# Kernel optimization log

Hardware: AMD Instinct MI355X
Metric: run time of the kernel (lower is better)

The kernel has to match this reference:

```python
import jax, jax.numpy as jnp
import numpy as np

HEADS = 16
DIM_HEAD = 64


def setup_inputs() -> dict:
    key = jax.random.key(0)
    k1, k2, k3, k4 = jax.random.split(key, 4)
    B, T, D = 4, 1024, 1024
    x = jax.random.normal(k1, (B, T, D), dtype=jnp.float32)
    w_qkv = jax.random.normal(k2, (3 * HEADS * DIM_HEAD, D), dtype=jnp.float32) * (1.0 / np.sqrt(D))
    w_out = jax.random.normal(k3, (D, HEADS * DIM_HEAD), dtype=jnp.float32) * (1.0 / np.sqrt(HEADS * DIM_HEAD))
    rel_bias = jax.random.normal(k4, (2 * 1024 - 1, HEADS), dtype=jnp.float32) * 0.02
    return {"x": x, "w_qkv": w_qkv, "w_out": w_out, "rel_bias": rel_bias}


def reference(x, w_qkv, w_out, rel_bias):
    b, t, _ = x.shape
    h, dh = HEADS, DIM_HEAD
    scale = dh ** (-0.5)
    qkv = x @ w_qkv.T  # [b, t, 3*h*dh]
    # einops 'b t (d k h) -> k b h t d': last axis factors as (dh, 3, h)
    qkv = qkv.reshape(b, t, dh, 3, h).transpose(3, 0, 4, 1, 2)  # [3, b, h, t, dh]
    q, k, v = qkv[0], qkv[1], qkv[2]
    scores = jnp.einsum('bhid,bhjd->bhij', q, k) * scale  # [b, h, t, t]
    # relative position bias: rel[i,j] = j - i + t - 1
    rel = jnp.arange(t)[None, :] - jnp.arange(t)[:, None] + (t - 1)  # [t, t]
    bias = rel_bias[rel]  # [t, t, h]
    scores = scores + bias.transpose(2, 0, 1)[None]  # [b, h, t, t]
    attn = jax.nn.softmax(scores, axis=-1)
    out = jnp.einsum('bhij,bhjd->bhid', attn, v)  # [b, h, t, dh]
    out = out.transpose(0, 2, 1, 3).reshape(b, t, h * dh)  # 'b h t d -> b t (h d)'
    return out @ w_out.T
```

## Files before the change

### kernel.cpp

```cpp
#include <hip/hip_runtime.h>
#include <hip/hip_bf16.h>

typedef short bf16x8 __attribute__((ext_vector_type(8)));
typedef float f32x4  __attribute__((ext_vector_type(4)));

typedef __attribute__((address_space(3))) void lds_t;
typedef __attribute__((address_space(1))) void gbl_t;

#define MFMA16(a,b,c) __builtin_amdgcn_mfma_f32_16x16x32_bf16((a),(b),(c),0,0,0)

__device__ __forceinline__ unsigned short f2bf(float f) {
    __hip_bfloat16 h = __float2bfloat16(f);
    return __builtin_bit_cast(unsigned short, h);
}
__device__ __forceinline__ float bf2f(unsigned short u) {
    __hip_bfloat16 h = __builtin_bit_cast(__hip_bfloat16, u);
    return __bfloat162float(h);
}

__global__ void prep_all(const float* __restrict__ x,
                         const float* __restrict__ w_qkv,
                         const float* __restrict__ w_out,
                         unsigned short* __restrict__ A1h,
                         unsigned short* __restrict__ W1h,
                         unsigned short* __restrict__ W3h) {
    const int NX = 4096 * 256, NW1 = 3072 * 256, NW3 = 1024 * 256;
    for (int idx = blockIdx.x * blockDim.x + threadIdx.x; idx < NX + NW1 + NW3;
         idx += gridDim.x * blockDim.x) {
        if (idx < NX) {
            int base = idx * 4;
            float4 v = *reinterpret_cast<const float4*>(x + base);
            ushort4 hi;
            hi.x = f2bf(v.x); hi.y = f2bf(v.y);
            hi.z = f2bf(v.z); hi.w = f2bf(v.w);
            *reinterpret_cast<ushort4*>(A1h + base) = hi;
        } else if (idx < NX + NW1) {
            int base = (idx - NX) * 4;
            int n = base >> 10, c = base & 1023;
            int d = n & 63, which = n >> 10, h = (n >> 6) & 15;
            int srow = d * 48 + which * 16 + h;
            float4 v =
                *reinterpret_cast<const float4*>(w_qkv + (size_t)srow * 1024 + c);
            ushort4 hi;
            hi.x = f2bf(v.x); hi.y = f2bf(v.y);
            hi.z = f2bf(v.z); hi.w = f2bf(v.w);
            *reinterpret_cast<ushort4*>(W1h + (size_t)n * 1024 + c) = hi;
        } else {
            int base = (idx - NX - NW1) * 4;
            float4 v = *reinterpret_cast<const float4*>(w_out + base);
            ushort4 hi;
            hi.x = f2bf(v.x); hi.y = f2bf(v.y);
            hi.z = f2bf(v.z); hi.w = f2bf(v.w);
            *reinterpret_cast<ushort4*>(W3h + base) = hi;
        }
    }
}

__global__ __launch_bounds__(512, 2) void gemm256_hi(
    const unsigned short* __restrict__ A, const unsigned short* __restrict__ B,
    unsigned short* __restrict__ outQ, unsigned short* __restrict__ outK,
    unsigned short* __restrict__ outV) {
    __shared__ unsigned short lds[65536];
    const int tid = threadIdx.x;
    const int wid = tid >> 6, lane = tid & 63;
    const int lrow = lane & 15, lgrp = lane >> 4;
    const int wr = wid >> 2, wc = wid & 3;
    const int mtile = blockIdx.y * 256, ntile = blockIdx.x * 256;

    const int csw = lgrp ^ ((lrow >> 1) & 3);
    const int aoff = (wr * 128 + lrow) * 32 + csw * 8;
    const int boff = 32768 + (wc * 64 + lrow) * 32 + csw * 8;

    const int sreg = wid * 2;
    const int srow0 = sreg * 16 + (lane >> 2);
    const int srow1 = (sreg + 1) * 16 + (lane >> 2);
    const int schunk = (lane & 3) ^ ((lane >> 3) & 3);
    const int sdst0 = sreg * 512;

    f32x4 acc[8][4];
#pragma unroll
    for (int i = 0; i < 8; ++i)
#pragma unroll
        for (int j = 0; j < 4; ++j) {
            f32x4 z = {0.f, 0.f, 0.f, 0.f};
            acc[i][j] = z;
        }

#pragma unroll
    for (int s0 = 0; s0 < 2; ++s0) {
        const int kb = s0 * 32;
        __builtin_amdgcn_global_load_lds(
            (const gbl_t*)(A + (size_t)(mtile + srow0) * 1024 + kb + schunk * 8),
            (lds_t*)(lds + s0 * 8192 + sdst0), 16, 0, 0);
        __builtin_amdgcn_global_load_lds(
            (const gbl_t*)(A + (size_t)(mtile + srow1) * 1024 + kb + schunk * 8),
            (lds_t*)(lds + s0 * 8192 + sdst0 + 512), 16, 0, 0);
        __builtin_amdgcn_global_load_lds(
            (const gbl_t*)(B + (size_t)(ntile + srow0) * 1024 + kb + schunk * 8),
            (lds_t*)(lds + 32768 + s0 * 8192 + sdst0), 16, 0, 0);
        __builtin_amdgcn_global_load_lds(
            (const gbl_t*)(B + (size_t)(ntile + srow1) * 1024 + kb + schunk * 8),
            (lds_t*)(lds + 32768 + s0 * 8192 + sdst0 + 512), 16, 0, 0);
    }
    asm volatile("s_waitcnt vmcnt(4)" ::: "memory");
    __syncthreads();

    for (int s = 0; s < 32; ++s) {
        const int sa = s & 3;
        const unsigned short* sbase = lds + sa * 8192;

        bf16x8 af[8];
#pragma unroll
        for (int i = 0; i < 8; ++i)
            af[i] = *reinterpret_cast<const bf16x8*>(sbase + aoff + i * 512);
        bf16x8 b0 = *reinterpret_cast<const bf16x8*>(sbase + boff);
        bf16x8 b1 = *reinterpret_cast<const bf16x8*>(sbase + boff + 512);

        if (s <= 29) {
            const int kb2 = (s + 2) * 32;
            const int s2 = (s + 2) & 3;
            __builtin_amdgcn_global_load_lds(
                (const gbl_t*)(A + (size_t)(mtile + srow0) * 1024 + kb2 + schunk * 8),
                (lds_t*)(lds + s2 * 8192 + sdst0), 16, 0, 0);
            __builtin_amdgcn_global_load_lds(
                (const gbl_t*)(A + (size_t)(mtile + srow1) * 1024 + kb2 + schunk * 8),
                (lds_t*)(lds + s2 * 8192 + sdst0 + 512), 16, 0, 0);
        }
        __builtin_amdgcn_s_setprio(1);
#pragma unroll
        for (int i = 0; i < 8; ++i) {
            acc[i][0] = MFMA16(af[i], b0, acc[i][0]);
            acc[i][1] = MFMA16(af[i], b1, acc[i][1]);
        }
        __builtin_amdgcn_s_setprio(0);

        bf16x8 b2 = *reinterpret_cast<const bf16x8*>(sbase + boff + 1024);
        bf16x8 b3 = *reinterpret_cast<const bf16x8*>(sbase + boff + 1536);
        if (s <= 29) {
            const int kb2 = (s + 2) * 32;
            const int s2 = (s + 2) & 3;
            __builtin_amdgcn_global_load_lds(
                (const gbl_t*)(B + (size_t)(ntile + srow0) * 1024 + kb2 + schunk * 8),
                (lds_t*)(lds + 32768 + s2 * 8192 + sdst0), 16, 0, 0);
            __builtin_amdgcn_global_load_lds(
                (const gbl_t*)(B + (size_t)(ntile + srow1) * 1024 + kb2 + schunk * 8),
                (lds_t*)(lds + 32768 + s2 * 8192 + sdst0 + 512), 16, 0, 0);
        }
        __builtin_amdgcn_s_setprio(1);
#pragma unroll
        for (int i = 0; i < 8; ++i) {
            acc[i][2] = MFMA16(af[i], b2, acc[i][2]);
            acc[i][3] = MFMA16(af[i], b3, acc[i][3]);
        }
        __builtin_amdgcn_s_setprio(0);

        if (s < 31) {
            if (s <= 29)
                asm volatile("s_waitcnt vmcnt(4)" ::: "memory");
            else
                asm volatile("s_waitcnt vmcnt(0)" ::: "memory");
            __syncthreads();
        }
    }

#pragma unroll
    for (int i = 0; i < 8; ++i) {
#pragma unroll
        for (int j = 0; j < 4; ++j) {
#pragma unroll
            for (int r = 0; r < 4; ++r) {
                float v = acc[i][j][r];
                int m = mtile + wr * 128 + i * 16 + lgrp * 4 + r;
                int n = ntile + wc * 64 + j * 16 + lrow;
                int which = n >> 10;
                int hh = (n >> 6) & 15;
                int d = n & 63;
                int b = m >> 10, t = m & 1023;
                unsigned short* dstp =
                    (which == 0) ? outQ : ((which == 1) ? outK : outV);
                dstp[((size_t)((b << 4) + hh) * 1024 + t) * 64 + d] = f2bf(v);
            }
        }
    }
}

__global__ __launch_bounds__(256, 3) void gemm_out_v5(
    const unsigned short* __restrict__ A, const unsigned short* __restrict__ B,
    float* __restrict__ outF) {
    __shared__ unsigned short As[2][64 * 64];
    __shared__ unsigned short Bs[2][128 * 64];
    const int tid = threadIdx.x;
    const int wid = tid >> 6, lane = tid & 63;
    const int lrow = lane & 15, lgrp = lane >> 4;
    const int wr = wid >> 1, wc = wid & 1;
    const int h = blockIdx.x;
    const int xcd = h & 7, within = h >> 3;
    const int mtile = (xcd * 8 + (within & 7)) * 64;
    const int ntile = (within >> 3) * 128;

    const int srow = tid >> 3;
    const int schunk = (tid & 7) ^ (srow & 7);
    const unsigned short* Abase = A + (size_t)(mtile + srow) * 1024 + schunk * 8;
    const unsigned short* Bbase = B + (size_t)(ntile + srow) * 1024 + schunk * 8;

    const int csw0 = (lgrp ^ (lrow & 7)) * 8;
    const int csw1 = ((4 | lgrp) ^ (lrow & 7)) * 8;
    const int arow = wr * 32 + lrow;
    const int brow = wc * 64 + lrow;

    f32x4 acc[2][4];
#pragma unroll
    for (int i = 0; i < 2; ++i)
#pragma unroll
        for (int j = 0; j < 4; ++j) {
            f32x4 z = {0.f, 0.f, 0.f, 0.f};
            acc[i][j] = z;
        }

#pragma unroll
    for (int e = 0; e < 2; ++e)
        __builtin_amdgcn_global_load_lds(
            (const gbl_t*)(Abase + (size_t)e * 32 * 1024),
            (lds_t*)(&As[0][0] + e * 2048 + tid * 8), 16, 0, 0);
#pragma unroll
    for (int e = 0; e < 4; ++e)
        __builtin_amdgcn_global_load_lds(
            (const gbl_t*)(Bbase + (size_t)e * 32 * 1024),
            (lds_t*)(&Bs[0][0] + e * 2048 + tid * 8), 16, 0, 0);
    asm volatile("s_waitcnt vmcnt(0)" ::: "memory");
    __syncthreads();

    for (int s = 0; s < 16; ++s) {
        const int cur = s & 1;
        if (s < 15) {
            const int kb = (s + 1) * 64;
            const int nx = cur ^ 1;
#pragma unroll
            for (int e = 0; e < 2; ++e)
                __builtin_amdgcn_global_load_lds(
                    (const gbl_t*)(Abase + (size_t)e * 32 * 1024 + kb),
                    (lds_t*)(&As[nx][0] + e * 2048 + tid * 8), 16, 0, 0);
#pragma unroll
            for (int e = 0; e < 4; ++e)
                __builtin_amdgcn_global_load_lds(
                    (const gbl_t*)(Bbase + (size_t)e * 32 * 1024 + kb),
                    (lds_t*)(&Bs[nx][0] + e * 2048 + tid * 8), 16, 0, 0);
        }
        bf16x8 a0[2], a1[2], b0[4], b1[4];
#pragma unroll
        for (int i = 0; i < 2; ++i) {
            a0[i] = *reinterpret_cast<const bf16x8*>(&As[cur][0] +
                                                     (arow + i * 16) * 64 + csw0);
            a1[i] = *reinterpret_cast<const bf16x8*>(&As[cur][0] +
                                                     (arow + i * 16) * 64 + csw1);
        }
#pragma unroll
        for (int j = 0; j < 4; ++j) {
            b0[j] = *reinterpret_cast<const bf16x8*>(&Bs[cur][0] +
                                                     (brow + j * 16) * 64 + csw0);
            b1[j] = *reinterpret_cast<const bf16x8*>(&Bs[cur][0] +
                                                     (brow + j * 16) * 64 + csw1);
        }
        __builtin_amdgcn_s_setprio(1);
#pragma unroll
        for (int i = 0; i < 2; ++i)
#pragma unroll
            for (int j = 0; j < 4; ++j) {
                acc[i][j] = MFMA16(a0[i], b0[j], acc[i][j]);
                acc[i][j] = MFMA16(a1[i], b1[j], acc[i][j]);
            }
        __builtin_amdgcn_s_setprio(0);
        if (s < 15) {
            asm volatile("s_waitcnt vmcnt(0)" ::: "memory");
            __syncthreads();
        }
    }

#pragma unroll
    for (int i = 0; i < 2; ++i)
#pragma unroll
        for (int j = 0; j < 4; ++j)
#pragma unroll
            for (int r = 0; r < 4; ++r) {
                int m = mtile + wr * 32 + i * 16 + lgrp * 4 + r;
                int n = ntile + wc * 64 + j * 16 + lrow;
                outF[(size_t)m * 1024 + n] = acc[i][j][r];
            }
}

__global__ __launch_bounds__(256) void transpose_v(
    const unsigned short* __restrict__ Vb, unsigned short* __restrict__ Vtg) {
    __shared__ unsigned short L[64][72];
    const int tt = blockIdx.x, bh = blockIdx.y;
    const int tid = threadIdx.x;
#pragma unroll
    for (int e = 0; e < 2; ++e) {
        int chunk = e * 256 + tid;
        int r = chunk >> 3, c = (chunk & 7) * 8;
        uint4 v = *reinterpret_cast<const uint4*>(
            Vb + ((size_t)bh * 1024 + tt * 64 + r) * 64 + c);
        *reinterpret_cast<uint4*>(&L[r][c]) = v;
    }
    __syncthreads();
#pragma unroll
    for (int e = 0; e < 2; ++e) {
        int chunk = e * 256 + tid;
        int d = chunk >> 3, t0 = (chunk & 7) * 8;
        unsigned short tmp[8];
#pragma unroll
        for (int u = 0; u < 8; ++u) tmp[u] = L[t0 + u][d];
        *reinterpret_cast<uint4*>(Vtg + ((size_t)bh * 64 + d) * 1024 + tt * 64 +
                                  t0) = *reinterpret_cast<const uint4*>(tmp);
    }
}

__global__ __launch_bounds__(512) void attn_kernel(
    const unsigned short* __restrict__ Qb, const unsigned short* __restrict__ Kb,
    const unsigned short* __restrict__ Vtg, const float* __restrict__ rel_bias,
    unsigned short* __restrict__ A3) {
    const int qt = blockIdx.x;
    const int bh = blockIdx.y;
    const int b = bh >> 4, h = bh & 15;
    const int tid = threadIdx.x;
    const int w = tid >> 6, lane = tid & 63;
    const int lrow = lane & 15, lgrp = lane >> 4;
    const float LOG2E = 1.4426950408889634f;
    const float SCALE2 = 0.125f * 1.4426950408889634f;
    const float THR = 11.5f;

    __shared__ unsigned short Ks[2][64 * 64];
    __shared__ unsigned short Vs[2][64 * 64];
    __shared__ unsigned short Ps[8][16 * 64];
    __shared__ float BiasF[1152];

    const unsigned short* Ktile = Kb + (size_t)bh * 1024 * 64;
    const unsigned short* Vtile = Vtg + (size_t)bh * 64 * 1024;

    const unsigned short* Qp =
        Qb + ((size_t)bh * 1024 + qt * 128 + w * 16 + lrow) * 64;
    bf16x8 qa0 = *reinterpret_cast<const bf16x8*>(Qp + lgrp * 8);
    bf16x8 qa1 = *reinterpret_cast<const bf16x8*>(Qp + 32 + lgrp * 8);

    const int sr0 = w * 8 + (lane >> 3);
    const int sc_lo = lane & 7;

    float m_run = -3.0e38f;
    float l_run = 0.f;
    f32x4 o_acc[4];
#pragma unroll
    for (int n = 0; n < 4; n++) {
        f32x4 z = {0.f, 0.f, 0.f, 0.f};
        o_acc[n] = z;
    }

    const int bbase = lgrp * 4 + 127 - w * 16 - lrow;

    {
        {
            int r = sr0;
            int c = sc_lo ^ (r & 7);
            __builtin_amdgcn_global_load_lds(
                (const gbl_t*)(Ktile + (size_t)r * 64 + c * 8),
                (lds_t*)(&Ks[0][0] + w * 512), 16, 0, 0);
            __builtin_amdgcn_global_load_lds(
                (const gbl_t*)(Vtile + (size_t)r * 1024 + c * 8),
                (lds_t*)(&Vs[0][0] + w * 512), 16, 0, 0);
        }
        const int rbase = 896 - qt * 128;
        for (int t = tid; t < 1151; t += 512)
            BiasF[t] = rel_bias[(size_t)(t + rbase) * 16 + h] * LOG2E;
        asm volatile("s_waitcnt vmcnt(0)" ::: "memory");
        __syncthreads();
    }

    for (int kv = 0; kv < 16; ++kv) {
        const int cur = kv & 1;
        const int j0 = kv * 64;
        if (kv < 15) {
            const int j0n = (kv + 1) * 64;
            int r = sr0;
            int c = sc_lo ^ (r & 7);
            __builtin_amdgcn_global_load_lds(
                (const gbl_t*)(Ktile + (size_t)(j0n + r) * 64 + c * 8),
                (lds_t*)(&Ks[cur ^ 1][0] + w * 512), 16, 0, 0);
            __builtin_amdgcn_global_load_lds(
                (const gbl_t*)(Vtile + (size_t)r * 1024 + j0n + c * 8),
                (lds_t*)(&Vs[cur ^ 1][0] + w * 512), 16, 0, 0);
        }

        const unsigned short* kbuf = &Ks[cur][0];
        f32x4 s[4];
        __builtin_amdgcn_s_setprio(1);
#pragma unroll
        for (int f = 0; f < 4; ++f) {
            int krow = f * 16 + lrow;
            int sw0 = (lgrp ^ (lrow & 7)) * 8;
            int sw1 = ((4 | lgrp) ^ (lrow & 7)) * 8;
            bf16x8 kb0 = *reinterpret_cast<const bf16x8*>(kbuf + krow * 64 + sw0);
            bf16x8 kb1 = *reinterpret_cast<const bf16x8*>(kbuf + krow * 64 + sw1);
            f32x4 z = {0.f, 0.f, 0.f, 0.f};
            z = MFMA16(kb0, qa0, z);
            z = MFMA16(kb1, qa1, z);
            s[f] = z;
        }
        __builtin_amdgcn_s_setprio(0);

        float x[4][4];
        float pm = -3.0e38f;
#pragma unroll
        for (int f = 0; f < 4; ++f)
#pragma unroll
            for (int r = 0; r < 4; ++r) {
                float xv = s[f][r] * SCALE2 + BiasF[j0 + bbase + f * 16 + r];
                x[f][r] = xv;
                pm = fmaxf(pm, xv);
            }
        pm = fmaxf(pm, __shfl_xor(pm, 16));
        pm = fmaxf(pm, __shfl_xor(pm, 32));

        if (!__all(pm - m_run <= THR)) {
            float mnew = fmaxf(m_run, pm);
            float corr = __builtin_amdgcn_exp2f(m_run - mnew);
            m_run = mnew;
            l_run *= corr;
            float cb[4];
#pragma unroll
            for (int r = 0; r < 4; ++r) cb[r] = __shfl(corr, lgrp * 4 + r);
#pragma unroll
            for (int n = 0; n < 4; n++)
#pragma unroll
                for (int r = 0; r < 4; r++) o_acc[n][r] *= cb[r];
        }

        float su = 0.f;
#pragma unroll
        for (int f = 0; f < 4; ++f)
#pragma unroll
            for (int r = 0; r < 4; ++r) {
                float pv = __builtin_amdgcn_exp2f(x[f][r] - m_run);
                x[f][r] = pv;
                su += pv;
            }
        l_run += su;

#pragma unroll
        for (int f = 0; f < 4; ++f) {
            unsigned int plo, phi;
            asm("v_cvt_pk_bf16_f32 %0, %1, %2"
                : "=v"(plo)
                : "v"(x[f][0]), "v"(x[f][1]));
            asm("v_cvt_pk_bf16_f32 %0, %1, %2"
                : "=v"(phi)
                : "v"(x[f][2]), "v"(x[f][3]));
            const int chunk = (f * 2 + (lgrp >> 1)) ^ (lrow & 7);
            uint2 pw;
            pw.x = plo;
            pw.y = phi;
            *reinterpret_cast<uint2*>(
                &Ps[w][lrow * 64 + chunk * 8 + (lgrp & 1) * 4]) = pw;
        }

        const unsigned short* vbuf = &Vs[cur][0];
        __builtin_amdgcn_s_setprio(1);
#pragma unroll
        for (int jc = 0; jc < 2; ++jc) {
            int pc = ((4 * jc + lgrp) ^ (lrow & 7)) * 8;
            bf16x8 pa =
                *reinterpret_cast<const bf16x8*>(&Ps[w][0] + lrow * 64 + pc);
#pragma unroll
            for (int n = 0; n < 4; n++) {
                int vrow = n * 16 + lrow;
                bf16x8 vb =
                    *reinterpret_cast<const bf16x8*>(vbuf + vrow * 64 + pc);
                o_acc[n] = MFMA16(pa, vb, o_acc[n]);
            }
        }
        __builtin_amdgcn_s_setprio(0);

        if (kv < 15) {
            asm volatile("s_waitcnt vmcnt(0)" ::: "memory");
            __syncthreads();
        }
    }

    float lt = l_run + __shfl_xor(l_run, 16);
    lt += __shfl_xor(lt, 32);
    float rl[4];
#pragma unroll
    for (int r = 0; r < 4; ++r) rl[r] = 1.0f / __shfl(lt, lgrp * 4 + r);

#pragma unroll
    for (int n = 0; n < 4; n++) {
#pragma unroll
        for (int r = 0; r < 4; r++) {
            float val = o_acc[n][r] * rl[r];
            int ia = qt * 128 + w * 16 + lgrp * 4 + r;
            size_t m = (size_t)b * 1024 + ia;
            int col = h * 64 + n * 16 + lrow;
            A3[m * 1024 + col] = f2bf(val);
        }
    }
}

extern "C" void kernel_launch(void* const* d_in, const int* in_sizes, int n_in,
                              void* d_out, int out_size, void* d_ws,
                              size_t ws_size, hipStream_t stream) {
    const float* x = (const float*)d_in[0];
    const float* w_qkv = (const float*)d_in[1];
    const float* w_out = (const float*)d_in[2];
    const float* rel_bias = (const float*)d_in[3];
    float* out = (float*)d_out;

    char* ws = (char*)d_ws;
    size_t off = 0;
    auto alloc = [&](size_t bytes) {
        char* p = ws + off;
        off += (bytes + 255) & ~(size_t)255;
        return p;
    };
    unsigned short* A1h = (unsigned short*)alloc((size_t)4096 * 1024 * 2);
    unsigned short* W1h = (unsigned short*)alloc((size_t)3072 * 1024 * 2);
    unsigned short* Qb = (unsigned short*)alloc((size_t)64 * 1024 * 64 * 2);
    unsigned short* Kb = (unsigned short*)alloc((size_t)64 * 1024 * 64 * 2);
    unsigned short* Vb = (unsigned short*)alloc((size_t)64 * 1024 * 64 * 2);
    unsigned short* A3h = (unsigned short*)alloc((size_t)4096 * 1024 * 2);
    unsigned short* W3h = (unsigned short*)alloc((size_t)1024 * 1024 * 2);
    unsigned short* Vtg = A1h;

    hipLaunchKernelGGL(prep_all, dim3(2048), dim3(256), 0, stream, x, w_qkv,
                       w_out, A1h, W1h, W3h);
    hipLaunchKernelGGL(gemm256_hi, dim3(12, 16), dim3(512), 0, stream, A1h, W1h,
                       Qb, Kb, Vb);
    hipLaunchKernelGGL(transpose_v, dim3(16, 64), dim3(256), 0, stream, Vb, Vtg);
    hipLaunchKernelGGL(attn_kernel, dim3(8, 64), dim3(512), 0, stream, Qb, Kb,
                       Vtg, rel_bias, A3h);
    hipLaunchKernelGGL(gemm_out_v5, dim3(512), dim3(256), 0, stream, A3h, W3h,
                       out);
}
```

Measured before the change: 105.2 us.

## Restructure QKV GEMM to BK=64 double-buffered pipeline with XOR-8 swizzle

Reworks the QKV projection GEMM main loop from a 4-stage ring of 32-wide K slices (prefetch distance 2) into a 2-buffer scheme with 64-wide K slices, halving barrier count. The LDS layout changes to 64-element rows with an 8-way XOR swizzle, and each thread now loads whole rows with simpler addressing. Launch bounds drop to one block per SM. The trade-off is a shallower prefetch with a full vmcnt(0) wait each iteration, plus possibly lower occupancy, against fewer syncs and larger MFMA bursts.

New measurement: 101.2 us. 3.8% less time.

```diff
diff --git a/kernel.cpp b/kernel.cpp
--- a/kernel.cpp
+++ b/kernel.cpp
@@ -56,7 +56,7 @@
     }
 }
 
-__global__ __launch_bounds__(512, 2) void gemm256_hi(
+__global__ __launch_bounds__(512, 1) void gemm256_hi(
     const unsigned short* __restrict__ A, const unsigned short* __restrict__ B,
     unsigned short* __restrict__ outQ, unsigned short* __restrict__ outK,
     unsigned short* __restrict__ outV) {
@@ -67,15 +67,17 @@
     const int wr = wid >> 2, wc = wid & 3;
     const int mtile = blockIdx.y * 256, ntile = blockIdx.x * 256;
 
-    const int csw = lgrp ^ ((lrow >> 1) & 3);
-    const int aoff = (wr * 128 + lrow) * 32 + csw * 8;
-    const int boff = 32768 + (wc * 64 + lrow) * 32 + csw * 8;
-
-    const int sreg = wid * 2;
-    const int srow0 = sreg * 16 + (lane >> 2);
-    const int srow1 = (sreg + 1) * 16 + (lane >> 2);
-    const int schunk = (lane & 3) ^ ((lane >> 3) & 3);
-    const int sdst0 = sreg * 512;
+    const int csw0 = (lgrp ^ (lrow & 7)) * 8;
+    const int csw1 = ((4 | lgrp) ^ (lrow & 7)) * 8;
+    const int arowb = (wr * 128 + lrow) * 64;
+    const int browb = (wc * 64 + lrow) * 64;
+
+    const int srow = tid >> 3;
+    const int schunk = tid & 7;
+    const int gchunk = schunk ^ (srow & 7);
+    const unsigned short* Abase = A + (size_t)(mtile + srow) * 1024 + gchunk * 8;
+    const unsigned short* Bbase = B + (size_t)(ntile + srow) * 1024 + gchunk * 8;
+    const int sdst = srow * 64 + schunk * 8;
 
     f32x4 acc[8][4];
 #pragma unroll
@@ -87,78 +89,79 @@
         }
 
 #pragma unroll
-    for (int s0 = 0; s0 < 2; ++s0) {
-        const int kb = s0 * 32;
+    for (int e = 0; e < 4; ++e)
         __builtin_amdgcn_global_load_lds(
-            (const gbl_t*)(A + (size_t)(mtile + srow0) * 1024 + kb + schunk * 8),
-            (lds_t*)(lds + s0 * 8192 + sdst0), 16, 0, 0);
+            (const gbl_t*)(Abase + (size_t)e * 64 * 1024),
+            (lds_t*)(lds + e * 4096 + sdst), 16, 0, 0);
+#pragma unroll
+    for (int e = 0; e < 4; ++e)
         __builtin_amdgcn_global_load_lds(
-            (const gbl_t*)(A + (size_t)(mtile + srow1) * 1024 + kb + schunk * 8),
-            (lds_t*)(lds + s0 * 8192 + sdst0 + 512), 16, 0, 0);
-        __builtin_amdgcn_global_load_lds(
-            (const gbl_t*)(B + (size_t)(ntile + srow0) * 1024 + kb + schunk * 8),
-            (lds_t*)(lds + 32768 + s0 * 8192 + sdst0), 16, 0, 0);
-        __builtin_amdgcn_global_load_lds(
-            (const gbl_t*)(B + (size_t)(ntile + srow1) * 1024 + kb + schunk * 8),
-            (lds_t*)(lds + 32768 + s0 * 8192 + sdst0 + 512), 16, 0, 0);
-    }
-    asm volatile("s_waitcnt vmcnt(4)" ::: "memory");
+            (const gbl_t*)(Bbase + (size_t)e * 64 * 1024),
+            (lds_t*)(lds + 32768 + e * 4096 + sdst), 16, 0, 0);
+    asm volatile("s_waitcnt vmcnt(0)" ::: "memory");
     __syncthreads();
 
-    for (int s = 0; s < 32; ++s) {
-        const int sa = s & 3;
-        const unsigned short* sbase = lds + sa * 8192;
-
-        bf16x8 af[8];
-#pragma unroll
-        for (int i = 0; i < 8; ++i)
-            af[i] = *reinterpret_cast<const bf16x8*>(sbase + aoff + i * 512);
-        bf16x8 b0 = *reinterpret_cast<const bf16x8*>(sbase + boff);
-        bf16x8 b1 = *reinterpret_cast<const bf16x8*>(sbase + boff + 512);
-
-        if (s <= 29) {
-            const int kb2 = (s + 2) * 32;
-            const int s2 = (s + 2) & 3;
-            __builtin_amdgcn_global_load_lds(
-                (const gbl_t*)(A + (size_t)(mtile + srow0) * 1024 + kb2 + schunk * 8),
-                (lds_t*)(lds + s2 * 8192 + sdst0), 16, 0, 0);
-            __builtin_amdgcn_global_load_lds(
-                (const gbl_t*)(A + (size_t)(mtile + srow1) * 1024 + kb2 + schunk * 8),
-                (lds_t*)(lds + s2 * 8192 + sdst0 + 512), 16, 0, 0);
-        }
-        __builtin_amdgcn_s_setprio(1);
-#pragma unroll
-        for (int i = 0; i < 8; ++i) {
-            acc[i][0] = MFMA16(af[i], b0, acc[i][0]);
-            acc[i][1] = MFMA16(af[i], b1, acc[i][1]);
-        }
-        __builtin_amdgcn_s_setprio(0);
-
-        bf16x8 b2 = *reinterpret_cast<const bf16x8*>(sbase + boff + 1024);
-        bf16x8 b3 = *reinterpret_cast<const bf16x8*>(sbase + boff + 1536);
-        if (s <= 29) {
-            const int kb2 = (s + 2) * 32;
-            const int s2 = (s + 2) & 3;
-            __builtin_amdgcn_global_load_lds(
-                (const gbl_t*)(B + (size_t)(ntile + srow0) * 1024 + kb2 + schunk * 8),
-                (lds_t*)(lds + 32768 + s2 * 8192 + sdst0), 16, 0, 0);
-            __builtin_amdgcn_global_load_lds(
-                (const gbl_t*)(B + (size_t)(ntile + srow1) * 1024 + kb2 + schunk * 8),
-                (lds_t*)(lds + 32768 + s2 * 8192 + sdst0 + 512), 16, 0, 0);
-        }
-        __builtin_amdgcn_s_setprio(1);
-#pragma unroll
-        for (int i = 0; i < 8; ++i) {
-            acc[i][2] = MFMA16(af[i], b2, acc[i][2]);
-            acc[i][3] = MFMA16(af[i], b3, acc[i][3]);
-        }
-        __builtin_amdgcn_s_setprio(0);
-
-        if (s < 31) {
-            if (s <= 29)
-                asm volatile("s_waitcnt vmcnt(4)" ::: "memory");
-            else
-                asm volatile("s_waitcnt vmcnt(0)" ::: "memory");
+    for (int s = 0; s < 16; ++s) {
+        const int cur = s & 1;
+        const unsigned short* abuf = lds + cur * 16384;
+        const unsigned short* bbuf = lds + 32768 + cur * 16384;
+        const int nx = cur ^ 1;
+        const int kb = (s + 1) * 64;
+
+        if (s < 15) {
+#pragma unroll
+            for (int e = 0; e < 4; ++e)
+                __builtin_amdgcn_global_load_lds(
+                    (const gbl_t*)(Abase + (size_t)e * 64 * 1024 + kb),
+                    (lds_t*)(lds + nx * 16384 + e * 4096 + sdst), 16, 0, 0);
+        }
+        {
+            bf16x8 af[8], bfv[4];
+#pragma unroll
+            for (int i = 0; i < 8; ++i)
+                af[i] = *reinterpret_cast<const bf16x8*>(abuf + arowb + i * 1024 +
+                                                         csw0);
+#pragma unroll
+            for (int j = 0; j < 4; ++j)
+                bfv[j] = *reinterpret_cast<const bf16x8*>(bbuf + browb +
+                                                          j * 1024 + csw0);
+            __builtin_amdgcn_s_setprio(1);
+#pragma unroll
+            for (int i = 0; i < 8; ++i)
+#pragma unroll
+                for (int j = 0; j < 4; ++j)
+                    acc[i][j] = MFMA16(af[i], bfv[j], acc[i][j]);
+            __builtin_amdgcn_s_setprio(0);
+        }
+        if (s < 15) {
+#pragma unroll
+            for (int e = 0; e < 4; ++e)
+                __builtin_amdgcn_global_load_lds(
+                    (const gbl_t*)(Bbase + (size_t)e * 64 * 1024 + kb),
+                    (lds_t*)(lds + 32768 + nx * 16384 + e * 4096 + sdst), 16, 0,
+                    0);
+        }
+        {
+            bf16x8 af[8], bfv[4];
+#pragma unroll
+            for (int i = 0; i < 8; ++i)
+                af[i] = *reinterpret_cast<const bf16x8*>(abuf + arowb + i * 1024 +
+                                                         csw1);
+#pragma unroll
+            for (int j = 0; j < 4; ++j)
+                bfv[j] = *reinterpret_cast<const bf16x8*>(bbuf + browb +
+                                                          j * 1024 + csw1);
+            __builtin_amdgcn_s_setprio(1);
+#pragma unroll
+            for (int i = 0; i < 8; ++i)
+#pragma unroll
+                for (int j = 0; j < 4; ++j)
+                    acc[i][j] = MFMA16(af[i], bfv[j], acc[i][j]);
+            __builtin_amdgcn_s_setprio(0);
+        }
+
+        if (s < 15) {
+            asm volatile("s_waitcnt vmcnt(0)" ::: "memory");
             __syncthreads();
         }
     }
```
